# Performance work log

Measured on AMD Instinct MI355X. Metric: run time of the kernel, lower is better.

The kernel has to match this reference:

```python
import jax, jax.numpy as jnp
import numpy as np

N = 100000
E = 1_600_000
DIN = 24
DH = 64
DOUT = 12
NEG_SLOPE = 0.01  # torch F.leaky_relu default


def setup_inputs() -> dict:
    key = jax.random.key(0)
    ks = jax.random.split(key, 18)
    inp = {}
    inp["feats"] = jax.random.normal(ks[0], (N, DIN), dtype=jnp.float32)
    inp["e_w"] = jax.random.uniform(ks[1], (E, 1), dtype=jnp.float32)
    inp["snorm_n"] = jnp.ones((N, 1), dtype=jnp.float32)
    inp["snorm_e"] = jnp.ones((E, 1), dtype=jnp.float32)
    inp["src"] = jax.random.randint(ks[2], (E,), 0, N, dtype=jnp.int32)
    inp["dst"] = jax.random.randint(ks[3], (E,), 0, N, dtype=jnp.int32)
    s = 0.05
    inp["emb_h_W"] = jax.random.normal(ks[4], (DH, DIN), dtype=jnp.float32) * s
    inp["emb_h_b"] = jnp.zeros((DH,), dtype=jnp.float32)
    inp["emb_e_W"] = jax.random.normal(ks[5], (DH, 1), dtype=jnp.float32) * s
    inp["emb_e_b"] = jnp.zeros((DH,), dtype=jnp.float32)
    inp["W_self1"] = jax.random.normal(ks[6], (DH, DH), dtype=jnp.float32) * s
    inp["W_func1"] = jax.random.normal(ks[7], (DH, DH), dtype=jnp.float32) * s
    inp["attn1"] = jax.random.normal(ks[8], (3 * DH,), dtype=jnp.float32) * s
    inp["W_self2"] = jax.random.normal(ks[9], (DH, DH), dtype=jnp.float32) * s
    inp["W_func2"] = jax.random.normal(ks[10], (DH, DH), dtype=jnp.float32) * s
    inp["attn2"] = jax.random.normal(ks[11], (3 * DH,), dtype=jnp.float32) * s
    inp["lin1_W"] = jax.random.normal(ks[12], (DOUT, DH), dtype=jnp.float32) * s
    inp["lin1_b"] = jnp.zeros((DOUT,), dtype=jnp.float32)
    return inp


def _gat_layer(h, w_edge, src, dst, W_self, W_func, attn):
    # h: [N, d], w_edge: [E, d] edge embedding, attn: [3d]
    h_s = h @ W_self.T                       # linear_self(h)
    z = h @ W_func.T                         # linear_func(h)
    d = z.shape[-1]
    a_src, a_dst, a_w = attn[:d], attn[d:2 * d], attn[2 * d:]
    # attention score: W_a . [z_src, z_dst, w]  (decomposed to avoid [E,3d] concat)
    s_node_src = z @ a_src                   # [N]
    s_node_dst = z @ a_dst                   # [N]
    e = s_node_src[src] + s_node_dst[dst] + w_edge @ a_w  # [E]
    e = jax.nn.leaky_relu(e, NEG_SLOPE)
    # segment softmax over incoming edges per destination node
    m = jax.ops.segment_max(e, dst, num_segments=h.shape[0])
    ex = jnp.exp(e - m[dst])
    denom = jax.ops.segment_sum(ex, dst, num_segments=h.shape[0])
    alpha = ex / denom[dst]                  # [E]
    msg = alpha[:, None] * z[src]            # [E, d]
    agg = jax.ops.segment_sum(msg, dst, num_segments=h.shape[0])  # [N, d]
    # DGL: nodes with no incoming edges keep their old 'h' (not h_s + agg)
    in_deg = jax.ops.segment_sum(jnp.ones_like(e), dst, num_segments=h.shape[0])
    h_mid = jnp.where((in_deg > 0)[:, None], h_s + agg, h)
    return h + jax.nn.relu(h_mid)            # relu then residual


def reference(feats, e_w, snorm_n, snorm_e, src, dst,
              emb_h_W, emb_h_b, emb_e_W, emb_e_b,
              W_self1, W_func1, attn1, W_self2, W_func2, attn2,
              lin1_W, lin1_b):
    feats = feats.reshape(feats.shape[0], -1)
    h = feats @ emb_h_W.T + emb_h_b          # [N, DH]
    e = e_w @ emb_e_W.T + emb_e_b            # [E, DH]
    h = _gat_layer(h, e, src, dst, W_self1, W_func1, attn1)
    h = _gat_layer(h, e, src, dst, W_self2, W_func2, attn2)
    y = h @ lin1_W.T + lin1_b                # [N, DOUT]
    return y
```

## Files before the change

### kernel.cpp

```cpp
#include <hip/hip_runtime.h>
#include <hip/hip_fp16.h>

#define N_NODES 100000
#define N_EDGES 1600000
#define DIN 24
#define DH 64
#define DOUT 12
#define NEG_SLOPE 0.01f
#define NG 8
#define EPG (N_EDGES / NG)
#define NS 7
#define SLICE_N 16384
#define NTOT (NG * N_NODES)
#define SCAN_BLK 4096
#define LDSW 72

#define NB_HIST (NS * NG)
#define NB_EMBED ((N_NODES * DH) / 1024)
#define NB_SCAN1G ((NTOT + SCAN_BLK - 1) / SCAN_BLK)
#define NB_SUMDEG ((N_NODES + 255) / 256)
#define NB_SCAN1N ((N_NODES + SCAN_BLK - 1) / SCAN_BLK)
#define NB_SCAN3G ((NTOT + 255) / 256)
#define NB_SCATTER (NG * 128)
#define BPE ((EPG + 127) / 128)
#define NB_NODE ((N_NODES + 63) / 64)
#define NB_SCAN3N ((N_NODES + 255) / 256)
#define NB_COMPACT ((N_NODES + 31) / 32)
#define NB_AGG ((N_NODES + 7) / 8)

typedef _Float16 half8_t __attribute__((ext_vector_type(8)));
typedef float floatx4 __attribute__((ext_vector_type(4)));

__device__ __forceinline__ void dev_consts(const float* emb_e_W, const float* emb_e_b,
                                           const float* attn1, const float* attn2,
                                           float* consts) {
    int lane = threadIdx.x;
    if (lane >= 64) return;
    float w = emb_e_W[lane], b = emb_e_b[lane];
    float a1 = attn1[2 * DH + lane], a2 = attn2[2 * DH + lane];
    float c11 = w * a1, c01 = b * a1, c12 = w * a2, c02 = b * a2;
    for (int off = 32; off; off >>= 1) {
        c11 += __shfl_down(c11, off);
        c01 += __shfl_down(c01, off);
        c12 += __shfl_down(c12, off);
        c02 += __shfl_down(c02, off);
    }
    if (lane == 0) {
        consts[0] = c11; consts[1] = c01; consts[2] = c12; consts[3] = c02;
    }
}

__device__ __forceinline__ void dev_hist(int bid, const int* dst,
                                         unsigned char* deg, unsigned char* rank) {
    __shared__ unsigned cnt[SLICE_N / 4];
    int s = bid % NS, c = bid / NS;
    for (int i = threadIdx.x; i < SLICE_N / 4; i += 1024) cnt[i] = 0;
    __syncthreads();
    int nbase = s * SLICE_N;
    int start = c * EPG, end = start + EPG;
    for (int i = start + threadIdx.x; i < end; i += 1024) {
        int local = dst[i] - nbase;
        if ((unsigned)local < SLICE_N) {
            unsigned sh = (unsigned)(local & 3) * 8u;
            unsigned old = atomicAdd(&cnt[local >> 2], 1u << sh);
            rank[i] = (unsigned char)((old >> sh) & 255u);
        }
    }
    __syncthreads();
    const unsigned char* cb = (const unsigned char*)cnt;
    for (int l = threadIdx.x; l < SLICE_N; l += 1024) {
        int n = nbase + l;
        if (n < N_NODES) deg[c * N_NODES + n] = cb[l];
    }
}

__device__ __forceinline__ void dev_embed(int bid, const float* feats, const float* W,
                                          const float* b, float* h) {
    int idx = bid * 1024 + threadIdx.x;
    if (idx >= N_NODES * DH) return;
    int n = idx >> 6, o = idx & 63;
    const float* f = feats + n * DIN;
    const float* w = W + o * DIN;
    float acc = b[o];
#pragma unroll
    for (int k = 0; k < DIN; ++k) acc += f[k] * w[k];
    h[idx] = acc;
}

__device__ __forceinline__ void dev_scan1B(int bid, const unsigned* inW, int* out,
                                           int* part, int n) {
    __shared__ int lds[256];
    int t = threadIdx.x;
    int base = bid * SCAN_BLK + t * 16;
    unsigned wv[4];
#pragma unroll
    for (int i = 0; i < 4; ++i) wv[i] = inW[(base >> 2) + i];
    int v[16];
    int s = 0;
#pragma unroll
    for (int i = 0; i < 16; ++i) {
        int idx = base + i;
        int c = (int)((wv[i >> 2] >> ((i & 3) * 8)) & 255u);
        v[i] = (idx < n) ? c : 0;
        s += v[i];
    }
    lds[t] = s;
    __syncthreads();
    for (int off = 1; off < 256; off <<= 1) {
        int y = (t >= off) ? lds[t - off] : 0;
        __syncthreads();
        lds[t] += y;
        __syncthreads();
    }
    int run = lds[t] - s;
#pragma unroll
    for (int i = 0; i < 16; ++i) {
        int idx = base + i;
        if (idx < n) out[idx] = run;
        run += v[i];
    }
    if (t == 255) part[bid] = lds[255];
}

__device__ __forceinline__ void dev_scan1(int bid, const int* in, int* out,
                                          int* part, int n) {
    __shared__ int lds[256];
    int t = threadIdx.x;
    int base = bid * SCAN_BLK + t * 16;
    int v[16];
    int s = 0;
#pragma unroll
    for (int i = 0; i < 16; ++i) {
        int idx = base + i;
        v[i] = (idx < n) ? in[idx] : 0;
        s += v[i];
    }
    lds[t] = s;
    __syncthreads();
    for (int off = 1; off < 256; off <<= 1) {
        int y = (t >= off) ? lds[t - off] : 0;
        __syncthreads();
        lds[t] += y;
        __syncthreads();
    }
    int run = lds[t] - s;
#pragma unroll
    for (int i = 0; i < 16; ++i) {
        int idx = base + i;
        if (idx < n) out[idx] = run;
        run += v[i];
    }
    if (t == 255) part[bid] = lds[255];
}

__device__ __forceinline__ void dev_scan2(int* part, int nblk) {
    __shared__ int lds2[256];
    int t = threadIdx.x;
    int orig = (t < nblk) ? part[t] : 0;
    lds2[t] = orig;
    __syncthreads();
    for (int off = 1; off < 256; off <<= 1) {
        int y = (t >= off) ? lds2[t - off] : 0;
        __syncthreads();
        lds2[t] += y;
        __syncthreads();
    }
    if (t < nblk) part[t] = lds2[t] - orig;
}

__device__ __forceinline__ void dev_sumdeg(int bid, const unsigned char* degB, int* degN) {
    int n = bid * 256 + threadIdx.x;
    if (n >= N_NODES) return;
    int s = 0;
#pragma unroll
    for (int g = 0; g < NG; ++g) s += (int)degB[g * N_NODES + n];
    degN[n] = s;
}

__device__ __forceinline__ void dev_scatter(int bid, const int* src, const int* dst,
                                            const float* e_w, const unsigned char* rank,
                                            const int* row_offG, unsigned* csr) {
    int g = bid & 7, q = bid >> 3;
    int start = g * EPG + q * BPE;
    int end = start + BPE;
    int gend = (g + 1) * EPG;
    if (end > gend) end = gend;
    const int* ro = row_offG + g * N_NODES;
    for (int i = start + threadIdx.x; i < end; i += 256) {
        int d = dst[i];
        unsigned qv = (unsigned)(e_w[i] * 32768.f);
        if (qv > 32767u) qv = 32767u;
        unsigned w = (unsigned)src[i] | (qv << 17);
        int pos = ro[d] + (int)rank[i];
        csr[pos] = w;
    }
}

__device__ __forceinline__ void dev_node(int bid, const float* h,
                                         const float* Wself, const float* Wfunc,
                                         const float* attn,
                                         __half* zh, float* hs,
                                         float* s_src, float* s_dst) {
    __shared__ _Float16 lds[2 * 64 * LDSW];
    int tid = threadIdx.x;
    for (int idx = tid; idx < 2 * 64 * 64; idx += 256) {
        int mat = idx >> 12, rem = idx & 4095;
        int o = rem >> 6, k = rem & 63;
        float v = mat ? Wfunc[rem] : Wself[rem];
        lds[(mat * 64 + o) * LDSW + k] = (_Float16)v;
    }
    __syncthreads();

    int wave = tid >> 6, lane = tid & 63;
    int n0 = (bid * 4 + wave) * 16;
    if (n0 >= N_NODES) return;
    int quad = lane >> 4, lm = lane & 15;

    half8_t afrag[2];
    {
        const float4* hrow = (const float4*)(h + (size_t)(n0 + lm) * DH);
#pragma unroll
        for (int ks = 0; ks < 2; ++ks) {
            float4 p0 = hrow[ks * 8 + quad * 2];
            float4 p1 = hrow[ks * 8 + quad * 2 + 1];
            half8_t a;
            a[0] = (_Float16)p0.x; a[1] = (_Float16)p0.y;
            a[2] = (_Float16)p0.z; a[3] = (_Float16)p0.w;
            a[4] = (_Float16)p1.x; a[5] = (_Float16)p1.y;
            a[6] = (_Float16)p1.z; a[7] = (_Float16)p1.w;
            afrag[ks] = a;
        }
    }

    floatx4 accS[4], accF[4];
#pragma unroll
    for (int t = 0; t < 4; ++t) { accS[t] = (floatx4)0.f; accF[t] = (floatx4)0.f; }

    const _Float16* bS = lds;
    const _Float16* bF = lds + 64 * LDSW;
#pragma unroll
    for (int t = 0; t < 4; ++t) {
        int o = t * 16 + lm;
#pragma unroll
        for (int ks = 0; ks < 2; ++ks) {
            int hoff = o * LDSW + ks * 32 + quad * 8;
            half8_t b1 = *(const half8_t*)(bS + hoff);
            half8_t b2 = *(const half8_t*)(bF + hoff);
            accS[t] = __builtin_amdgcn_mfma_f32_16x16x32_f16(afrag[ks], b1, accS[t], 0, 0, 0);
            accF[t] = __builtin_amdgcn_mfma_f32_16x16x32_f16(afrag[ks], b2, accF[t], 0, 0, 0);
        }
    }

    float asv[4], adv[4];
#pragma unroll
    for (int t = 0; t < 4; ++t) {
        asv[t] = attn[t * 16 + lm];
        adv[t] = attn[DH + t * 16 + lm];
    }
    float ps[4] = {0.f, 0.f, 0.f, 0.f}, pd[4] = {0.f, 0.f, 0.f, 0.f};
#pragma unroll
    for (int t = 0; t < 4; ++t) {
#pragma unroll
        for (int r = 0; r < 4; ++r) {
            int node = n0 + quad * 4 + r;
            float zv = accF[t][r];
            zh[(size_t)node * DH + t * 16 + lm] = __float2half(zv);
            hs[(size_t)node * DH + t * 16 + lm] = accS[t][r];
            ps[r] += zv * asv[t];
            pd[r] += zv * adv[t];
        }
    }
#pragma unroll
    for (int r = 0; r < 4; ++r) {
        float p1 = ps[r], p2 = pd[r];
        for (int off = 8; off; off >>= 1) {
            p1 += __shfl_xor(p1, off);
            p2 += __shfl_xor(p2, off);
        }
        if (lm == 0) {
            s_src[n0 + quad * 4 + r] = p1;
            s_dst[n0 + quad * 4 + r] = p2;
        }
    }
}

__global__ void __launch_bounds__(1024, 2)
k_fuse1(const float* __restrict__ feats, const float* __restrict__ emb_h_W,
        const float* __restrict__ emb_h_b, float* __restrict__ h,
        const int* __restrict__ dst, unsigned char* __restrict__ deg,
        unsigned char* __restrict__ rank,
        const float* __restrict__ emb_e_W, const float* __restrict__ emb_e_b,
        const float* __restrict__ attn1, const float* __restrict__ attn2,
        float* __restrict__ consts) {
    int bid = blockIdx.x;
    if (bid == 0) { dev_consts(emb_e_W, emb_e_b, attn1, attn2, consts); return; }
    bid -= 1;
    if (bid < NB_HIST) { dev_hist(bid, dst, deg, rank); return; }
    dev_embed(bid - NB_HIST, feats, emb_h_W, emb_h_b, h);
}

__global__ void k_fuse2(const unsigned* __restrict__ degW, int* __restrict__ row_offG,
                        int* __restrict__ partG, int* __restrict__ degN) {
    int bid = blockIdx.x;
    if (bid < NB_SCAN1G) { dev_scan1B(bid, degW, row_offG, partG, NTOT); return; }
    dev_sumdeg(bid - NB_SCAN1G, (const unsigned char*)degW, degN);
}

__global__ void k_fuse3(int* __restrict__ partG, const int* __restrict__ degN,
                        int* __restrict__ row_offN, int* __restrict__ partN) {
    int bid = blockIdx.x;
    if (bid == 0) { dev_scan2(partG, NB_SCAN1G); return; }
    dev_scan1(bid - 1, degN, row_offN, partN, N_NODES);
}

__global__ void k_fuse4(int* __restrict__ row_offG, const int* __restrict__ partG,
                        int* __restrict__ partN) {
    int bid = blockIdx.x;
    if (bid == 0) { dev_scan2(partN, NB_SCAN1N); return; }
    int i = (bid - 1) * 256 + threadIdx.x;
    if (i >= NTOT) return;
    row_offG[i] += partG[i / SCAN_BLK];
    if (i == 0) row_offG[NTOT] = N_EDGES;
}

__global__ void __launch_bounds__(256, 4)
k_fuse5(const int* __restrict__ src, const int* __restrict__ dst,
        const float* __restrict__ e_w, const unsigned char* __restrict__ rank,
        const int* __restrict__ row_offG, unsigned* __restrict__ csr,
        int* __restrict__ row_offN, const int* __restrict__ partN,
        const float* __restrict__ h, const float* __restrict__ Wself1,
        const float* __restrict__ Wfunc1, const float* __restrict__ attn1,
        __half* __restrict__ zh, float* __restrict__ hs,
        float* __restrict__ s_src, float* __restrict__ s_dst) {
    int bid = blockIdx.x;
    if (bid < NB_SCATTER) { dev_scatter(bid, src, dst, e_w, rank, row_offG, csr); return; }
    bid -= NB_SCATTER;
    if (bid < NB_NODE) { dev_node(bid, h, Wself1, Wfunc1, attn1, zh, hs, s_src, s_dst); return; }
    int i = (bid - NB_NODE) * 256 + threadIdx.x;
    if (i >= N_NODES) return;
    row_offN[i] += partN[i / SCAN_BLK];
    if (i == 0) row_offN[N_NODES] = N_EDGES;
}

__global__ void k_compact(const int* __restrict__ row_offG, const int* __restrict__ row_offN,
                          const unsigned* __restrict__ csr, unsigned* __restrict__ csr2) {
    int wave = threadIdx.x >> 6, lane = threadIdx.x & 63;
    int n0 = (blockIdx.x * 4 + wave) * 8;
    if (n0 >= N_NODES) return;
    int g = lane & 7, nl = lane >> 3;
    int n = n0 + nl;
    int offG = 0, dg = 0;
    if (n < N_NODES) {
        int idx = g * N_NODES + n;
        offG = row_offG[idx];
        dg = row_offG[idx + 1] - offG;
    }
    int x = dg;
#pragma unroll
    for (int s = 1; s < 8; s <<= 1) {
        int y = __shfl_up(x, s);
        if ((lane & 7) >= s) x += y;
    }
    if (n < N_NODES) {
        int base = row_offN[n] + (x - dg);
        for (int j = 0; j < dg; ++j) csr2[base + j] = csr[offG + j];
    }
}

__global__ void __launch_bounds__(256, 4)
k_nodeL(const float* __restrict__ h, const float* __restrict__ Wself,
        const float* __restrict__ Wfunc, const float* __restrict__ attn,
        __half* __restrict__ zh, float* __restrict__ hs,
        float* __restrict__ s_src, float* __restrict__ s_dst) {
    dev_node(blockIdx.x, h, Wself, Wfunc, attn, zh, hs, s_src, s_dst);
}

__global__ void k_agg(const int* __restrict__ row_off, const unsigned* __restrict__ csr,
                      const float* __restrict__ s_src, const float* __restrict__ s_dstA,
                      const float* __restrict__ consts, int layer,
                      const __half* __restrict__ zh, const float* __restrict__ hsb,
                      float* __restrict__ h,
                      const float* __restrict__ lin_W, const float* __restrict__ lin_b,
                      float* __restrict__ y, int final_layer) {
    int wave = threadIdx.x >> 6, lane = threadIdx.x & 63;
    int half = lane >> 5, hl = lane & 31;
    int eg = (lane >> 3) & 3, c8 = lane & 7;
    int n = blockIdx.x * 8 + wave * 2 + half;
    if (n >= N_NODES) return;
    int rs = row_off[n], deg = row_off[n + 1] - rs;
    int degO = __shfl_xor(deg, 32);
    int degmax = deg > degO ? deg : degO;

    float c1 = consts[layer * 2 + 0];
    float c0 = consts[layer * 2 + 1];
    float sd = s_dstA[n];

    float acc[8];
#pragma unroll
    for (int k = 0; k < 8; ++k) acc[k] = 0.f;
    float ssl = 0.f;
    int lbase = lane & 32;

    for (int base = 0; base < degmax; base += 32) {
        float ex = 0.f;
        int s0 = 0;
        int idx = base + hl;
        if (idx < deg) {
            unsigned w = csr[rs + idx];
            s0 = (int)(w & 0x1FFFFu);
            float ew = (float)(w >> 17) * (1.f / 32768.f);
            float e = s_src[s0] + sd + ew * c1 + c0;
            e = (e > 0.f) ? e : NEG_SLOPE * e;
            ex = __expf(e);
        }
        ssl += ex;
        int cnt = degmax - base;
        if (cnt > 32) cnt = 32;
#pragma unroll 4
        for (int jb = 0; jb < cnt; jb += 4) {
            int srcl = lbase + jb + eg;
            int sj = __shfl(s0, srcl);
            float exj = __shfl(ex, srcl);
            half8_t zv = *(const half8_t*)(zh + ((size_t)sj << 6) + (c8 << 3));
#pragma unroll
            for (int k = 0; k < 8; ++k) acc[k] += exj * (float)zv[k];
        }
    }
#pragma unroll
    for (int k = 0; k < 8; ++k) {
        acc[k] += __shfl_xor(acc[k], 8);
        acc[k] += __shfl_xor(acc[k], 16);
    }
    ssl += __shfl_xor(ssl, 16); ssl += __shfl_xor(ssl, 8);
    ssl += __shfl_xor(ssl, 4);  ssl += __shfl_xor(ssl, 2);
    ssl += __shfl_xor(ssl, 1);

    const float4* hp = (const float4*)(h + (size_t)n * DH);
    float4 ho0 = hp[c8 * 2], ho1 = hp[c8 * 2 + 1];
    float hold[8] = {ho0.x, ho0.y, ho0.z, ho0.w, ho1.x, ho1.y, ho1.z, ho1.w};
    float hnew[8];
    if (deg == 0) {
#pragma unroll
        for (int k = 0; k < 8; ++k) hnew[k] = hold[k] + fmaxf(hold[k], 0.f);
    } else {
        float rinv = 1.f / ssl;
        const float4* sp = (const float4*)(hsb + (size_t)n * DH);
        float4 hs0 = sp[c8 * 2], hs1 = sp[c8 * 2 + 1];
        float hsv[8] = {hs0.x, hs0.y, hs0.z, hs0.w, hs1.x, hs1.y, hs1.z, hs1.w};
#pragma unroll
        for (int k = 0; k < 8; ++k)
            hnew[k] = hold[k] + fmaxf(hsv[k] + acc[k] * rinv, 0.f);
    }

    if (!final_layer) {
        if (eg == 0) {
            float4* op = (float4*)(h + (size_t)n * DH);
            op[c8 * 2]     = make_float4(hnew[0], hnew[1], hnew[2], hnew[3]);
            op[c8 * 2 + 1] = make_float4(hnew[4], hnew[5], hnew[6], hnew[7]);
        }
    } else {
#pragma unroll
        for (int t = 0; t < 3; ++t) {
            int o = eg * 3 + t;
            const float* wr = lin_W + o * DH + c8 * 8;
            float p = 0.f;
#pragma unroll
            for (int k = 0; k < 8; ++k) p += hnew[k] * wr[k];
            p += __shfl_xor(p, 1); p += __shfl_xor(p, 2); p += __shfl_xor(p, 4);
            if (c8 == 0) y[n * DOUT + o] = p + lin_b[o];
        }
    }
}

extern "C" void kernel_launch(void* const* d_in, const int* in_sizes, int n_in,
                              void* d_out, int out_size, void* d_ws, size_t ws_size,
                              hipStream_t stream) {
    const float* feats   = (const float*)d_in[0];
    const float* e_w     = (const float*)d_in[1];
    const int*   src     = (const int*)d_in[4];
    const int*   dst     = (const int*)d_in[5];
    const float* emb_h_W = (const float*)d_in[6];
    const float* emb_h_b = (const float*)d_in[7];
    const float* emb_e_W = (const float*)d_in[8];
    const float* emb_e_b = (const float*)d_in[9];
    const float* Wself[2] = {(const float*)d_in[10], (const float*)d_in[13]};
    const float* Wfunc[2] = {(const float*)d_in[11], (const float*)d_in[14]};
    const float* attn[2]  = {(const float*)d_in[12], (const float*)d_in[15]};
    const float* lin1_W  = (const float*)d_in[16];
    const float* lin1_b  = (const float*)d_in[17];
    float* y = (float*)d_out;

    char* ws = (char*)d_ws;
    size_t off = 0;
    auto alloc = [&](size_t bytes) {
        void* p = ws + off;
        off += (bytes + 255) & ~(size_t)255;
        return p;
    };
    float*         h        = (float*)alloc((size_t)N_NODES * DH * 4);
    __half*        zh       = (__half*)alloc((size_t)N_NODES * DH * 2);
    float*         hs       = (float*)alloc((size_t)N_NODES * DH * 4);
    unsigned*      csr      = (unsigned*)alloc((size_t)N_EDGES * 4);
    unsigned*      csr2     = (unsigned*)alloc((size_t)N_EDGES * 4);
    float*         s_src    = (float*)alloc((size_t)N_NODES * 4);
    float*         s_dst    = (float*)alloc((size_t)N_NODES * 4);
    int*           row_offG = (int*)alloc((size_t)(NTOT + 1) * 4);
    int*           row_offN = (int*)alloc((size_t)(N_NODES + 1) * 4);
    unsigned char* deg      = (unsigned char*)alloc((size_t)NTOT + 8192);
    unsigned char* rank     = (unsigned char*)alloc((size_t)N_EDGES);
    int*           degN     = (int*)alloc((size_t)N_NODES * 4);
    int*           partG    = (int*)alloc(256 * 4);
    int*           partN    = (int*)alloc(256 * 4);
    float*         consts   = (float*)alloc(4 * 4);

    k_fuse1<<<1 + NB_HIST + NB_EMBED, 1024, 0, stream>>>(feats, emb_h_W, emb_h_b, h,
                                                         dst, deg, rank, emb_e_W, emb_e_b,
                                                         attn[0], attn[1], consts);
    k_fuse2<<<NB_SCAN1G + NB_SUMDEG, 256, 0, stream>>>((const unsigned*)deg, row_offG,
                                                       partG, degN);
    k_fuse3<<<1 + NB_SCAN1N, 256, 0, stream>>>(partG, degN, row_offN, partN);
    k_fuse4<<<1 + NB_SCAN3G, 256, 0, stream>>>(row_offG, partG, partN);
    k_fuse5<<<NB_SCATTER + NB_NODE + NB_SCAN3N, 256, 0, stream>>>(
        src, dst, e_w, rank, row_offG, csr, row_offN, partN,
        h, Wself[0], Wfunc[0], attn[0], zh, hs, s_src, s_dst);
    k_compact<<<NB_COMPACT, 256, 0, stream>>>(row_offG, row_offN, csr, csr2);
    k_agg<<<NB_AGG, 256, 0, stream>>>(row_offN, csr2, s_src, s_dst, consts, 0,
                                      zh, hs, h, lin1_W, lin1_b, y, 0);
    k_nodeL<<<NB_NODE, 256, 0, stream>>>(h, Wself[1], Wfunc[1], attn[1],
                                         zh, hs, s_src, s_dst);
    k_agg<<<NB_AGG, 256, 0, stream>>>(row_offN, csr2, s_src, s_dst, consts, 1,
                                      zh, hs, h, lin1_W, lin1_b, y, 1);
}
```

Measured before the change: 344.7 us.

## Split edges into 32 groups with 16-bit group-relative row offsets

```diff
diff --git a/kernel.cpp b/kernel.cpp
--- a/kernel.cpp
+++ b/kernel.cpp
@@ -7,7 +7,7 @@
 #define DH 64
 #define DOUT 12
 #define NEG_SLOPE 0.01f
-#define NG 8
+#define NG 32
 #define EPG (N_EDGES / NG)
 #define NS 7
 #define SLICE_N 16384
@@ -21,11 +21,11 @@
 #define NB_SUMDEG ((N_NODES + 255) / 256)
 #define NB_SCAN1N ((N_NODES + SCAN_BLK - 1) / SCAN_BLK)
 #define NB_SCAN3G ((NTOT + 255) / 256)
-#define NB_SCATTER (NG * 128)
-#define BPE ((EPG + 127) / 128)
+#define NB_SCATTER (NG * 32)
+#define BPE ((EPG + 31) / 32)
 #define NB_NODE ((N_NODES + 63) / 64)
 #define NB_SCAN3N ((N_NODES + 255) / 256)
-#define NB_COMPACT ((N_NODES + 31) / 32)
+#define NB_COMPACT ((N_NODES + 7) / 8)
 #define NB_AGG ((N_NODES + 7) / 8)
 
 typedef _Float16 half8_t __attribute__((ext_vector_type(8)));
@@ -67,11 +67,10 @@
         }
     }
     __syncthreads();
-    const unsigned char* cb = (const unsigned char*)cnt;
-    for (int l = threadIdx.x; l < SLICE_N; l += 1024) {
-        int n = nbase + l;
-        if (n < N_NODES) deg[c * N_NODES + n] = cb[l];
-    }
+    int nmax = N_NODES - nbase;
+    if (nmax > SLICE_N) nmax = SLICE_N;
+    unsigned* dw = (unsigned*)(deg + (size_t)c * N_NODES + nbase);
+    for (int l = threadIdx.x; l < (nmax >> 2); l += 1024) dw[l] = cnt[l];
 }
 
 __device__ __forceinline__ void dev_embed(int bid, const float* feats, const float* W,
@@ -87,8 +86,8 @@
     h[idx] = acc;
 }
 
-__device__ __forceinline__ void dev_scan1B(int bid, const unsigned* inW, int* out,
-                                           int* part, int n) {
+__device__ __forceinline__ void dev_scan1B(int bid, const unsigned* inW,
+                                           unsigned short* out, int* part, int n) {
     __shared__ int lds[256];
     int t = threadIdx.x;
     int base = bid * SCAN_BLK + t * 16;
@@ -116,7 +115,7 @@
 #pragma unroll
     for (int i = 0; i < 16; ++i) {
         int idx = base + i;
-        if (idx < n) out[idx] = run;
+        if (idx < n) out[idx] = (unsigned short)run;
         run += v[i];
     }
     if (t == 255) part[bid] = lds[255];
@@ -156,8 +155,15 @@
 __device__ __forceinline__ void dev_scan2(int* part, int nblk) {
     __shared__ int lds2[256];
     int t = threadIdx.x;
-    int orig = (t < nblk) ? part[t] : 0;
-    lds2[t] = orig;
+    int v[4];
+    int s = 0;
+#pragma unroll
+    for (int i = 0; i < 4; ++i) {
+        int idx = t * 4 + i;
+        v[i] = (idx < nblk) ? part[idx] : 0;
+        s += v[i];
+    }
+    lds2[t] = s;
     __syncthreads();
     for (int off = 1; off < 256; off <<= 1) {
         int y = (t >= off) ? lds2[t - off] : 0;
@@ -165,7 +171,13 @@
         lds2[t] += y;
         __syncthreads();
     }
-    if (t < nblk) part[t] = lds2[t] - orig;
+    int run = lds2[t] - s;
+#pragma unroll
+    for (int i = 0; i < 4; ++i) {
+        int idx = t * 4 + i;
+        if (idx < nblk) part[idx] = run;
+        run += v[i];
+    }
 }
 
 __device__ __forceinline__ void dev_sumdeg(int bid, const unsigned char* degB, int* degN) {
@@ -173,25 +185,26 @@
     if (n >= N_NODES) return;
     int s = 0;
 #pragma unroll
-    for (int g = 0; g < NG; ++g) s += (int)degB[g * N_NODES + n];
+    for (int g = 0; g < NG; ++g) s += (int)degB[(size_t)g * N_NODES + n];
     degN[n] = s;
 }
 
 __device__ __forceinline__ void dev_scatter(int bid, const int* src, const int* dst,
                                             const float* e_w, const unsigned char* rank,
-                                            const int* row_offG, unsigned* csr) {
-    int g = bid & 7, q = bid >> 3;
+                                            const unsigned short* row_offG, unsigned* csr) {
+    int g = bid & 31, q = bid >> 5;
     int start = g * EPG + q * BPE;
     int end = start + BPE;
     int gend = (g + 1) * EPG;
     if (end > gend) end = gend;
-    const int* ro = row_offG + g * N_NODES;
+    const unsigned short* ro = row_offG + (size_t)g * N_NODES;
+    int cbase = g * EPG;
     for (int i = start + threadIdx.x; i < end; i += 256) {
         int d = dst[i];
         unsigned qv = (unsigned)(e_w[i] * 32768.f);
         if (qv > 32767u) qv = 32767u;
         unsigned w = (unsigned)src[i] | (qv << 17);
-        int pos = ro[d] + (int)rank[i];
+        int pos = cbase + (int)ro[d] + (int)rank[i];
         csr[pos] = w;
     }
 }
@@ -299,7 +312,7 @@
     dev_embed(bid - NB_HIST, feats, emb_h_W, emb_h_b, h);
 }
 
-__global__ void k_fuse2(const unsigned* __restrict__ degW, int* __restrict__ row_offG,
+__global__ void k_fuse2(const unsigned* __restrict__ degW, unsigned short* __restrict__ row_offG,
                         int* __restrict__ partG, int* __restrict__ degN) {
     int bid = blockIdx.x;
     if (bid < NB_SCAN1G) { dev_scan1B(bid, degW, row_offG, partG, NTOT); return; }
@@ -313,20 +326,21 @@
     dev_scan1(bid - 1, degN, row_offN, partN, N_NODES);
 }
 
-__global__ void k_fuse4(int* __restrict__ row_offG, const int* __restrict__ partG,
+__global__ void k_fuse4(unsigned short* __restrict__ row_offG, const int* __restrict__ partG,
                         int* __restrict__ partN) {
     int bid = blockIdx.x;
     if (bid == 0) { dev_scan2(partN, NB_SCAN1N); return; }
     int i = (bid - 1) * 256 + threadIdx.x;
     if (i >= NTOT) return;
-    row_offG[i] += partG[i / SCAN_BLK];
-    if (i == 0) row_offG[NTOT] = N_EDGES;
+    int c = i / N_NODES;
+    int v = (int)row_offG[i] + partG[i >> 12] - c * EPG;
+    row_offG[i] = (unsigned short)v;
 }
 
 __global__ void __launch_bounds__(256, 4)
 k_fuse5(const int* __restrict__ src, const int* __restrict__ dst,
         const float* __restrict__ e_w, const unsigned char* __restrict__ rank,
-        const int* __restrict__ row_offG, unsigned* __restrict__ csr,
+        const unsigned short* __restrict__ row_offG, unsigned* __restrict__ csr,
         int* __restrict__ row_offN, const int* __restrict__ partN,
         const float* __restrict__ h, const float* __restrict__ Wself1,
         const float* __restrict__ Wfunc1, const float* __restrict__ attn1,
@@ -342,24 +356,26 @@
     if (i == 0) row_offN[N_NODES] = N_EDGES;
 }
 
-__global__ void k_compact(const int* __restrict__ row_offG, const int* __restrict__ row_offN,
+__global__ void k_compact(const unsigned short* __restrict__ row_offG,
+                          const unsigned char* __restrict__ degB,
+                          const int* __restrict__ row_offN,
                           const unsigned* __restrict__ csr, unsigned* __restrict__ csr2) {
     int wave = threadIdx.x >> 6, lane = threadIdx.x & 63;
-    int n0 = (blockIdx.x * 4 + wave) * 8;
+    int n0 = (blockIdx.x * 4 + wave) * 2;
     if (n0 >= N_NODES) return;
-    int g = lane & 7, nl = lane >> 3;
+    int g = lane & 31, nl = lane >> 5;
     int n = n0 + nl;
     int offG = 0, dg = 0;
     if (n < N_NODES) {
-        int idx = g * N_NODES + n;
-        offG = row_offG[idx];
-        dg = row_offG[idx + 1] - offG;
+        size_t idx = (size_t)g * N_NODES + n;
+        offG = g * EPG + (int)row_offG[idx];
+        dg = (int)degB[idx];
     }
     int x = dg;
 #pragma unroll
-    for (int s = 1; s < 8; s <<= 1) {
+    for (int s = 1; s < 32; s <<= 1) {
         int y = __shfl_up(x, s);
-        if ((lane & 7) >= s) x += y;
+        if ((lane & 31) >= s) x += y;
     }
     if (n < N_NODES) {
         int base = row_offN[n] + (x - dg);
@@ -497,21 +513,21 @@
         off += (bytes + 255) & ~(size_t)255;
         return p;
     };
-    float*         h        = (float*)alloc((size_t)N_NODES * DH * 4);
-    __half*        zh       = (__half*)alloc((size_t)N_NODES * DH * 2);
-    float*         hs       = (float*)alloc((size_t)N_NODES * DH * 4);
-    unsigned*      csr      = (unsigned*)alloc((size_t)N_EDGES * 4);
-    unsigned*      csr2     = (unsigned*)alloc((size_t)N_EDGES * 4);
-    float*         s_src    = (float*)alloc((size_t)N_NODES * 4);
-    float*         s_dst    = (float*)alloc((size_t)N_NODES * 4);
-    int*           row_offG = (int*)alloc((size_t)(NTOT + 1) * 4);
-    int*           row_offN = (int*)alloc((size_t)(N_NODES + 1) * 4);
-    unsigned char* deg      = (unsigned char*)alloc((size_t)NTOT + 8192);
-    unsigned char* rank     = (unsigned char*)alloc((size_t)N_EDGES);
-    int*           degN     = (int*)alloc((size_t)N_NODES * 4);
-    int*           partG    = (int*)alloc(256 * 4);
-    int*           partN    = (int*)alloc(256 * 4);
-    float*         consts   = (float*)alloc(4 * 4);
+    float*          h        = (float*)alloc((size_t)N_NODES * DH * 4);
+    __half*         zh       = (__half*)alloc((size_t)N_NODES * DH * 2);
+    float*          hs       = (float*)alloc((size_t)N_NODES * DH * 4);
+    unsigned*       csr      = (unsigned*)alloc((size_t)N_EDGES * 4);
+    unsigned*       csr2     = (unsigned*)alloc((size_t)N_EDGES * 4);
+    float*          s_src    = (float*)alloc((size_t)N_NODES * 4);
+    float*          s_dst    = (float*)alloc((size_t)N_NODES * 4);
+    unsigned short* row_offG = (unsigned short*)alloc((size_t)(NTOT + 128) * 2);
+    int*            row_offN = (int*)alloc((size_t)(N_NODES + 1) * 4);
+    unsigned char*  deg      = (unsigned char*)alloc((size_t)NTOT + 8192);
+    unsigned char*  rank     = (unsigned char*)alloc((size_t)N_EDGES);
+    int*            degN     = (int*)alloc((size_t)N_NODES * 4);
+    int*            partG    = (int*)alloc(1024 * 4);
+    int*            partN    = (int*)alloc(1024 * 4);
+    float*          consts   = (float*)alloc(4 * 4);
 
     k_fuse1<<<1 + NB_HIST + NB_EMBED, 1024, 0, stream>>>(feats, emb_h_W, emb_h_b, h,
                                                          dst, deg, rank, emb_e_W, emb_e_b,
@@ -523,7 +539,7 @@
     k_fuse5<<<NB_SCATTER + NB_NODE + NB_SCAN3N, 256, 0, stream>>>(
         src, dst, e_w, rank, row_offG, csr, row_offN, partN,
         h, Wself[0], Wfunc[0], attn[0], zh, hs, s_src, s_dst);
-    k_compact<<<NB_COMPACT, 256, 0, stream>>>(row_offG, row_offN, csr, csr2);
+    k_compact<<<NB_COMPACT, 256, 0, stream>>>(row_offG, deg, row_offN, csr, csr2);
     k_agg<<<NB_AGG, 256, 0, stream>>>(row_offN, csr2, s_src, s_dst, consts, 0,
                                       zh, hs, h, lin1_W, lin1_b, y, 0);
     k_nodeL<<<NB_NODE, 256, 0, stream>>>(h, Wself[1], Wfunc[1], attn[1],
```

Result: no change. 345.4 us (+0.2%).
